# Optimization experiments

Measured on AMD Instinct MI355X. Metric: run time of the kernel, lower is better.

## Reference

```python
import jax, jax.numpy as jnp
import numpy as np

C, M, D, B, BG_KNN = 8, 2048, 2048, 256, 50
TEMP, MOMENTUM = 0.05, 0.2


def setup_inputs() -> dict:
    key = jax.random.key(0)
    k1, k2, k3, k4 = jax.random.split(key, 4)
    inputs = jax.random.normal(k1, (B, D), jnp.float32)
    inputs = inputs / jnp.linalg.norm(inputs, axis=1, keepdims=True)  # ReID feats are L2-normed
    em = jax.random.normal(k2, (C * M, D), jnp.float32)
    em = em / jnp.linalg.norm(em, axis=1, keepdims=True)  # memory rows are kept unit-norm
    targets = jax.random.randint(k3, (B,), 0, M)          # global pseudo labels in [0, M)
    cams = jax.random.randint(k4, (B,), 0, C).astype(jnp.int32)
    return {"inputs": inputs, "em": em, "targets": targets, "cams": cams, "epoch": 6}


def _loss(inputs, em_sg, targets, cams, epoch):
    em3 = em_sg.reshape(C, M, D)
    loss = jnp.zeros((), jnp.float32)
    # per-camera intra-camera cross entropy (ExemplarMemory fwd: inputs @ em.T / temp)
    for cc in range(C):
        mask = (cams == cc)
        cnt = jnp.maximum(mask.sum(), 1).astype(jnp.float32)
        logits = (inputs @ em3[cc].T) / TEMP                       # [B, M]
        logp = jax.nn.log_softmax(logits, axis=1)
        ce = -jnp.take_along_axis(logp, targets[:, None], axis=1)[:, 0]
        loss = loss + jnp.where(mask.any(), jnp.where(mask, ce, 0.0).sum() / cnt, 0.0)
    if epoch >= 5:
        sims = inputs @ em_sg.T                                    # [B, C*M]
        # positives: one proxy per camera at row target + M*c
        pos_ind = targets[:, None] + M * jnp.arange(C)[None, :]    # [B, C]
        pos_logits = jnp.take_along_axis(sims, pos_ind, axis=1) / TEMP
        masked = jax.lax.stop_gradient(sims).at[jnp.arange(B)[:, None], pos_ind].set(-1000.0)
        _, neg_ind = jax.lax.top_k(masked, BG_KNN)                 # bg_knn hard negatives
        neg_logits = jnp.take_along_axis(sims, neg_ind, axis=1) / TEMP
        cat = jnp.concatenate([pos_logits, neg_logits], axis=1)   # [B, C+BG_KNN]
        logp = jax.nn.log_softmax(cat, axis=1)
        al = -logp[:, :C].mean(axis=1)                             # weights 1/#pos on positives
        for cc in range(C):
            mask = (cams == cc)
            cnt = jnp.maximum(mask.sum(), 1).astype(jnp.float32)
            loss = loss + jnp.where(mask.any(), 0.5 * jnp.where(mask, al, 0.0).sum() / cnt, 0.0)
    return loss


def reference(inputs, em, targets, cams, epoch):
    em_sg = jax.lax.stop_gradient(em)  # memory is a buffer: no grad flows to it in torch
    loss = _loss(inputs, em_sg, targets, cams, int(epoch))
    # sequential per-sample EMA scatter update + renorm (torch does this in backward)
    rows = cams.astype(jnp.int32) * M + targets.astype(jnp.int32)
    x_sg = jax.lax.stop_gradient(inputs)

    def step(em_cur, xr):
        x, r = xr
        row = MOMENTUM * em_cur[r] + (1.0 - MOMENTUM) * x
        row = row / jnp.linalg.norm(row)
        return em_cur.at[r].set(row), None

    em_new, _ = jax.lax.scan(step, em_sg, (x_sg, rows))
    return loss, em_new
```

## Files before the change

### kernel.cpp

```cpp
#include <hip/hip_runtime.h>

#define Bn 256
#define Dk 2048
#define Cc 8
#define Mm 2048
#define Nn 16384
#define BG 50
#define INV_T 20.0f

typedef __attribute__((ext_vector_type(8))) short bf16x8;
typedef __attribute__((ext_vector_type(4))) float f32x4;

__device__ inline short f2bf(float f) {
  unsigned u = __builtin_bit_cast(unsigned, f);
  u = (u + 0x7fffu + ((u >> 16) & 1u)) >> 16;
  return (short)u;
}
__device__ inline unsigned f2ord(float f) {
  unsigned u = __builtin_bit_cast(unsigned, f);
  return (u & 0x80000000u) ? ~u : (u | 0x80000000u);
}
__device__ inline float ord2f(unsigned o) {
  unsigned u = (o & 0x80000000u) ? (o ^ 0x80000000u) : ~o;
  return __builtin_bit_cast(float, u);
}

__global__ __launch_bounds__(256) void prep_kernel(const int* __restrict__ cams,
                                                   const int* __restrict__ targets,
                                                   int* __restrict__ cnt,
                                                   int* __restrict__ rowArr,
                                                   int* __restrict__ first) {
  __shared__ int rs[Bn];
  __shared__ int lc[Cc];
  const int t = threadIdx.x;
  const int r = cams[t] * Mm + targets[t];
  rs[t] = r;
  if (t < Cc) lc[t] = 0;
  __syncthreads();
  atomicAdd(&lc[cams[t]], 1);
  __syncthreads();
  if (t < Cc) cnt[t] = lc[t];
  int fst = 1;
  for (int j = 0; j < t; ++j)
    if (rs[j] == r) fst = 0;
  rowArr[t] = r;
  first[t] = fst;
}

__global__ __launch_bounds__(256) void convert_kernel(const float* __restrict__ x,
                                                      short* __restrict__ a, int n4) {
  int i = blockIdx.x * 256 + threadIdx.x;
  if (i >= n4) return;
  float4 v = ((const float4*)x)[i];
  int row = i >> 9, j = i & 511;
  int kt = j >> 3, off = (j & 7) * 4;
  short4 h;
  h.x = f2bf(v.x); h.y = f2bf(v.y); h.z = f2bf(v.z); h.w = f2bf(v.w);
  *(short4*)(a + (size_t)kt * (Bn * 32) + row * 32 + off) = h;
}

#define SA 40
__global__ __launch_bounds__(512) void gemm_copy_kernel(const short* __restrict__ A,
                                                        const float* __restrict__ Em,
                                                        float* __restrict__ sims,
                                                        float* __restrict__ out_em) {
  __shared__ __align__(16) short As[2][Bn * SA];
  __shared__ __align__(16) short Bs[2][64 * SA];
  const int tid = threadIdx.x;
  const int nbase = blockIdx.x * 64;
  const int lane = tid & 63;
  const int w = tid >> 6, wm = w & 3, wn = w >> 2;
  const int lr = lane & 15, lq = lane >> 4;

  f32x4 acc[4][2];
#pragma unroll
  for (int mi = 0; mi < 4; ++mi)
#pragma unroll
    for (int ni = 0; ni < 2; ++ni) acc[mi][ni] = (f32x4)(0.0f);

  const int arow0 = tid >> 2, achk = (tid & 3) * 8;
  const int brow = tid >> 3, bcol = (tid & 7) * 4;
  const size_t bgo_base = (size_t)(nbase + brow) * Dk + bcol;

  uint4 aReg0, aReg1;
  float4 bReg;
  aReg0 = *(const uint4*)(A + tid * 8);
  aReg1 = *(const uint4*)(A + (tid + 512) * 8);
  bReg = *(const float4*)(Em + bgo_base);

  for (int kt = 0; kt < 64; ++kt) {
    short* as = As[kt & 1];
    short* bs = Bs[kt & 1];
    *(uint4*)(as + arow0 * SA + achk) = aReg0;
    *(uint4*)(as + (arow0 + 128) * SA + achk) = aReg1;
    short4 hb;
    hb.x = f2bf(bReg.x); hb.y = f2bf(bReg.y); hb.z = f2bf(bReg.z); hb.w = f2bf(bReg.w);
    *(short4*)(bs + brow * SA + bcol) = hb;
    {
      size_t go = bgo_base + (size_t)kt * 32;
      out_em[go + 0] = bReg.x;
      out_em[go + 1] = bReg.y;
      out_em[go + 2] = bReg.z;
      out_em[go + 3] = bReg.w;
    }
    __syncthreads();
    if (kt < 63) {
      const short* ap = A + (size_t)(kt + 1) * (Bn * 32);
      aReg0 = *(const uint4*)(ap + tid * 8);
      aReg1 = *(const uint4*)(ap + (tid + 512) * 8);
      bReg = *(const float4*)(Em + bgo_base + (size_t)(kt + 1) * 32);
    }
    bf16x8 af[4], bfr[2];
#pragma unroll
    for (int mi = 0; mi < 4; ++mi)
      af[mi] = *(const bf16x8*)(as + (wm * 64 + mi * 16 + lr) * SA + lq * 8);
#pragma unroll
    for (int ni = 0; ni < 2; ++ni)
      bfr[ni] = *(const bf16x8*)(bs + (wn * 32 + ni * 16 + lr) * SA + lq * 8);
#pragma unroll
    for (int mi = 0; mi < 4; ++mi)
#pragma unroll
      for (int ni = 0; ni < 2; ++ni)
        acc[mi][ni] = __builtin_amdgcn_mfma_f32_16x16x32_bf16(af[mi], bfr[ni], acc[mi][ni], 0, 0, 0);
  }
#pragma unroll
  for (int mi = 0; mi < 4; ++mi)
#pragma unroll
    for (int ni = 0; ni < 2; ++ni)
#pragma unroll
      for (int r = 0; r < 4; ++r) {
        int m = wm * 64 + mi * 16 + lq * 4 + r;
        int n = nbase + wn * 32 + ni * 16 + lr;
        sims[(size_t)m * Nn + n] = acc[mi][ni][r];
      }
}

__device__ inline float blockRedSumF(float v, float* red, int tid) {
#pragma unroll
  for (int off = 32; off; off >>= 1) v += __shfl_down(v, off, 64);
  if ((tid & 63) == 0) red[tid >> 6] = v;
  __syncthreads();
  float r = red[0] + red[1] + red[2] + red[3];
  __syncthreads();
  return r;
}
__device__ inline int blockRedSumI(int v, int* red, int tid) {
#pragma unroll
  for (int off = 32; off; off >>= 1) v += __shfl_down(v, off, 64);
  if ((tid & 63) == 0) red[tid >> 6] = v;
  __syncthreads();
  int r = red[0] + red[1] + red[2] + red[3];
  __syncthreads();
  return r;
}
__device__ inline float blockRedMaxF(float v, float* red, int tid) {
#pragma unroll
  for (int off = 32; off; off >>= 1) v = fmaxf(v, __shfl_down(v, off, 64));
  if ((tid & 63) == 0) red[tid >> 6] = v;
  __syncthreads();
  float r = fmaxf(fmaxf(red[0], red[1]), fmaxf(red[2], red[3]));
  __syncthreads();
  return r;
}
__device__ inline unsigned blockRedMaxU(unsigned v, unsigned* red, int tid) {
#pragma unroll
  for (int off = 32; off; off >>= 1) { unsigned o = __shfl_down(v, off, 64); v = o > v ? o : v; }
  if ((tid & 63) == 0) red[tid >> 6] = v;
  __syncthreads();
  unsigned r = red[0];
  r = red[1] > r ? red[1] : r; r = red[2] > r ? red[2] : r; r = red[3] > r ? red[3] : r;
  __syncthreads();
  return r;
}

__global__ __launch_bounds__(256) void loss_kernel(const float* __restrict__ sims,
                                                   const int* __restrict__ targets,
                                                   const int* __restrict__ cams,
                                                   const int* __restrict__ cnt,
                                                   const int* __restrict__ epoch,
                                                   float* __restrict__ lossPartial) {
  __shared__ float redf[4];
  __shared__ int redi[4];
  __shared__ unsigned redu[4];
  __shared__ unsigned pordS[Cc];
  const int b = blockIdx.x, t = threadIdx.x;

  uint4 uarr[16];
  {
    const float4* src = (const float4*)(sims + (size_t)b * Nn);
#pragma unroll
    for (int q = 0; q < 16; ++q) {
      float4 v = src[q * 256 + t];
      uarr[q].x = f2ord(v.x); uarr[q].y = f2ord(v.y);
      uarr[q].z = f2ord(v.z); uarr[q].w = f2ord(v.w);
    }
  }
  const int cam = cams[b], tgt = targets[b];
  const int cg = cnt[cam];
  const float invc = 1.0f / (float)(cg > 0 ? cg : 1);

  {
    const int owner = (tgt >> 2) & 255;
    if (t == owner) {
      const int slot = tgt & 3;
#pragma unroll
      for (int c = 0; c < Cc; ++c) {
        const int chunk = (tgt >> 10) + 2 * c;
        uint4 uc = uarr[0];
#pragma unroll
        for (int q = 1; q < 16; ++q)
          if (chunk == q) uc = uarr[q];
        unsigned po = uc.x;
        if (slot == 1) po = uc.y;
        else if (slot == 2) po = uc.z;
        else if (slot == 3) po = uc.w;
        pordS[c] = po;
      }
    }
  }
  __syncthreads();
  unsigned pord[Cc];
  float pv[Cc];
#pragma unroll
  for (int c = 0; c < Cc; ++c) { pord[c] = pordS[c]; pv[c] = ord2f(pord[c]); }

  float cv[8];
  {
    uint4 u0 = uarr[0], u1 = uarr[1];
#pragma unroll
    for (int q = 0; q < 16; ++q) {
      if (2 * cam == q) u0 = uarr[q];
      if (2 * cam + 1 == q) u1 = uarr[q];
    }
    cv[0] = ord2f(u0.x); cv[1] = ord2f(u0.y); cv[2] = ord2f(u0.z); cv[3] = ord2f(u0.w);
    cv[4] = ord2f(u1.x); cv[5] = ord2f(u1.y); cv[6] = ord2f(u1.z); cv[7] = ord2f(u1.w);
  }
  float lm = cv[0];
#pragma unroll
  for (int k = 1; k < 8; ++k) lm = fmaxf(lm, cv[k]);
  const float maxv = blockRedMaxF(lm, redf, t);
  float ls = 0.0f;
#pragma unroll
  for (int k = 0; k < 8; ++k) ls += __expf((cv[k] - maxv) * INV_T);
  const float sumexp = blockRedSumF(ls, redf, t);
  float total = (__logf(sumexp) + (maxv - pv[cam]) * INV_T) * invc;

  if (*epoch >= 5) {
    unsigned cur = 0u;
#pragma unroll 1
    for (int bit = 31; bit >= 0; --bit) {
      const unsigned cand = cur | (1u << bit);
      int c = 0;
#pragma unroll
      for (int q = 0; q < 16; ++q)
        c += (uarr[q].x >= cand) + (uarr[q].y >= cand) + (uarr[q].z >= cand) + (uarr[q].w >= cand);
      int ctot = blockRedSumI(c, redi, t);
#pragma unroll
      for (int cc2 = 0; cc2 < Cc; ++cc2) ctot -= (pord[cc2] >= cand);
      if (ctot >= BG) cur = cand;
    }
    int cg2 = 0;
#pragma unroll
    for (int q = 0; q < 16; ++q)
      cg2 += (uarr[q].x > cur) + (uarr[q].y > cur) + (uarr[q].z > cur) + (uarr[q].w > cur);
    int cgt = blockRedSumI(cg2, redi, t);
#pragma unroll
    for (int cc2 = 0; cc2 < Cc; ++cc2) cgt -= (pord[cc2] > cur);
    unsigned um = 0u;
#pragma unroll
    for (int q = 0; q < 16; ++q) {
      um = uarr[q].x > um ? uarr[q].x : um;
      um = uarr[q].y > um ? uarr[q].y : um;
      um = uarr[q].z > um ? uarr[q].z : um;
      um = uarr[q].w > um ? uarr[q].w : um;
    }
    const unsigned umax = blockRedMaxU(um, redu, t);
    const float m = ord2f(umax);
    const float v50 = ord2f(cur);
    float s = 0.0f;
#pragma unroll
    for (int q = 0; q < 16; ++q) {
      if (uarr[q].x > cur) s += __expf((ord2f(uarr[q].x) - m) * INV_T);
      if (uarr[q].y > cur) s += __expf((ord2f(uarr[q].y) - m) * INV_T);
      if (uarr[q].z > cur) s += __expf((ord2f(uarr[q].z) - m) * INV_T);
      if (uarr[q].w > cur) s += __expf((ord2f(uarr[q].w) - m) * INV_T);
    }
    float S = blockRedSumF(s, redf, t);
    float psum = 0.0f;
#pragma unroll
    for (int cc2 = 0; cc2 < Cc; ++cc2) {
      if (pord[cc2] > cur) S -= __expf((pv[cc2] - m) * INV_T);
      S += __expf((pv[cc2] - m) * INV_T);
      psum += pv[cc2];
    }
    S += (float)(BG - cgt) * __expf((v50 - m) * INV_T);
    const float lse = m * INV_T + __logf(S);
    const float al = lse - psum * (INV_T / 8.0f);
    total += 0.5f * al * invc;
  }
  if (t == 0) lossPartial[b] = total;
}

__global__ __launch_bounds__(256) void finalize_kernel(const float* __restrict__ lossPartial,
                                                       float* __restrict__ loss) {
  __shared__ float redf[4];
  const int t = threadIdx.x;
  float v = lossPartial[t];
  const float r = blockRedSumF(v, redf, t);
  if (t == 0) loss[0] = r;
}

__global__ __launch_bounds__(256) void ema_kernel(const float* __restrict__ em,
                                                  const float* __restrict__ inputs,
                                                  const int* __restrict__ rowArr,
                                                  const int* __restrict__ first,
                                                  float* __restrict__ out_em) {
  const int b = blockIdx.x, tid = threadIdx.x;
  if (!first[b]) return;
  const int r = rowArr[b];
  __shared__ int rows[Bn];
  __shared__ float red[4];
  rows[tid] = rowArr[tid];
  __syncthreads();
  float v[8];
#pragma unroll
  for (int u = 0; u < 8; ++u) v[u] = em[(size_t)r * Dk + u * 256 + tid];
  const int lane = tid & 63, w = tid >> 6;
  for (int j = b; j < Bn; ++j) {
    if (rows[j] != r) continue;
#pragma unroll
    for (int u = 0; u < 8; ++u)
      v[u] = 0.2f * v[u] + 0.8f * inputs[(size_t)j * Dk + u * 256 + tid];
    float ss = 0.0f;
#pragma unroll
    for (int u = 0; u < 8; ++u) ss += v[u] * v[u];
#pragma unroll
    for (int off = 32; off; off >>= 1) ss += __shfl_down(ss, off, 64);
    if (lane == 0) red[w] = ss;
    __syncthreads();
    const float inv = 1.0f / sqrtf(red[0] + red[1] + red[2] + red[3]);
#pragma unroll
    for (int u = 0; u < 8; ++u) v[u] *= inv;
    __syncthreads();
  }
#pragma unroll
  for (int u = 0; u < 8; ++u) out_em[(size_t)r * Dk + u * 256 + tid] = v[u];
}

extern "C" void kernel_launch(void* const* d_in, const int* in_sizes, int n_in,
                              void* d_out, int out_size, void* d_ws, size_t ws_size,
                              hipStream_t stream) {
  const float* inputs  = (const float*)d_in[0];
  const float* em      = (const float*)d_in[1];
  const int*   targets = (const int*)d_in[2];
  const int*   cams    = (const int*)d_in[3];
  const int*   epoch   = (const int*)d_in[4];
  float* loss   = (float*)d_out;
  float* out_em = (float*)d_out + 1;

  float* sims = (float*)d_ws;
  short* a16  = (short*)((char*)d_ws + (size_t)Bn * Nn * 4);
  float* lossPartial = (float*)((char*)d_ws + (size_t)Bn * Nn * 4 + (size_t)Bn * Dk * 2);
  int* ibase  = (int*)(lossPartial + Bn);
  int* cnt    = ibase;
  int* rowArr = ibase + 8;
  int* first  = ibase + 8 + Bn;

  hipLaunchKernelGGL(prep_kernel,    dim3(1),       dim3(256), 0, stream, cams, targets, cnt, rowArr, first);
  hipLaunchKernelGGL(convert_kernel, dim3(512),     dim3(256), 0, stream, inputs, a16, Bn * Dk / 4);
  hipLaunchKernelGGL(gemm_copy_kernel, dim3(Nn / 64), dim3(512), 0, stream, a16, em, sims, out_em);
  hipLaunchKernelGGL(loss_kernel,    dim3(Bn),      dim3(256), 0, stream, sims, targets, cams, cnt, epoch, lossPartial);
  hipLaunchKernelGGL(finalize_kernel, dim3(1),      dim3(256), 0, stream, lossPartial, loss);
  hipLaunchKernelGGL(ema_kernel,     dim3(Bn),      dim3(256), 0, stream, em, inputs, rowArr, first, out_em);
}
```

Before: 370.4 us.

## Load GEMM fragments directly from global memory, dropping LDS staging and barriers

The GEMM+copy kernel no longer stages A and B tiles through shared memory with double buffering and __syncthreads. Each wave now loads its MFMA fragments straight from global memory (pre-tiled bf16 A, fp32 Em converted to bf16 in registers), and the loop is unrolled by 4 so loads can be issued ahead. This removes the LDS writes, reads and per-iteration barriers. In exchange, A and B data are fetched redundantly across waves: each A fragment is read by both wn waves and each B row by all four wm waves, which raises global/L2 traffic. The out_em copy stays as a separate stream of loads and stores.

Measured after the change: 407.8 us. 10.1% more time.

```diff
diff --git a/kernel.cpp b/kernel.cpp
--- a/kernel.cpp
+++ b/kernel.cpp
@@ -59,13 +59,10 @@
   *(short4*)(a + (size_t)kt * (Bn * 32) + row * 32 + off) = h;
 }
 
-#define SA 40
 __global__ __launch_bounds__(512) void gemm_copy_kernel(const short* __restrict__ A,
                                                         const float* __restrict__ Em,
                                                         float* __restrict__ sims,
                                                         float* __restrict__ out_em) {
-  __shared__ __align__(16) short As[2][Bn * SA];
-  __shared__ __align__(16) short Bs[2][64 * SA];
   const int tid = threadIdx.x;
   const int nbase = blockIdx.x * 64;
   const int lane = tid & 63;
@@ -78,51 +75,43 @@
 #pragma unroll
     for (int ni = 0; ni < 2; ++ni) acc[mi][ni] = (f32x4)(0.0f);
 
-  const int arow0 = tid >> 2, achk = (tid & 3) * 8;
-  const int brow = tid >> 3, bcol = (tid & 7) * 4;
-  const size_t bgo_base = (size_t)(nbase + brow) * Dk + bcol;
-
-  uint4 aReg0, aReg1;
-  float4 bReg;
-  aReg0 = *(const uint4*)(A + tid * 8);
-  aReg1 = *(const uint4*)(A + (tid + 512) * 8);
-  bReg = *(const float4*)(Em + bgo_base);
-
+  const short* aP = A + (wm * 64 + lr) * 32 + lq * 8;
+  const float* bP = Em + (size_t)(nbase + wn * 32 + lr) * Dk + lq * 8;
+  const int crow = tid >> 3, ccol = (tid & 7) * 4;
+  const float* cS = Em + (size_t)(nbase + crow) * Dk + ccol;
+  float* cD = out_em + (size_t)(nbase + crow) * Dk + ccol;
+
+#pragma unroll 4
   for (int kt = 0; kt < 64; ++kt) {
-    short* as = As[kt & 1];
-    short* bs = Bs[kt & 1];
-    *(uint4*)(as + arow0 * SA + achk) = aReg0;
-    *(uint4*)(as + (arow0 + 128) * SA + achk) = aReg1;
-    short4 hb;
-    hb.x = f2bf(bReg.x); hb.y = f2bf(bReg.y); hb.z = f2bf(bReg.z); hb.w = f2bf(bReg.w);
-    *(short4*)(bs + brow * SA + bcol) = hb;
-    {
-      size_t go = bgo_base + (size_t)kt * 32;
-      out_em[go + 0] = bReg.x;
-      out_em[go + 1] = bReg.y;
-      out_em[go + 2] = bReg.z;
-      out_em[go + 3] = bReg.w;
-    }
-    __syncthreads();
-    if (kt < 63) {
-      const short* ap = A + (size_t)(kt + 1) * (Bn * 32);
-      aReg0 = *(const uint4*)(ap + tid * 8);
-      aReg1 = *(const uint4*)(ap + (tid + 512) * 8);
-      bReg = *(const float4*)(Em + bgo_base + (size_t)(kt + 1) * 32);
-    }
-    bf16x8 af[4], bfr[2];
-#pragma unroll
-    for (int mi = 0; mi < 4; ++mi)
-      af[mi] = *(const bf16x8*)(as + (wm * 64 + mi * 16 + lr) * SA + lq * 8);
-#pragma unroll
-    for (int ni = 0; ni < 2; ++ni)
-      bfr[ni] = *(const bf16x8*)(bs + (wn * 32 + ni * 16 + lr) * SA + lq * 8);
-#pragma unroll
-    for (int mi = 0; mi < 4; ++mi)
-#pragma unroll
-      for (int ni = 0; ni < 2; ++ni)
-        acc[mi][ni] = __builtin_amdgcn_mfma_f32_16x16x32_bf16(af[mi], bfr[ni], acc[mi][ni], 0, 0, 0);
-  }
+    bf16x8 a0 = *(const bf16x8*)(aP + (size_t)kt * 8192);
+    bf16x8 a1 = *(const bf16x8*)(aP + (size_t)kt * 8192 + 512);
+    bf16x8 a2 = *(const bf16x8*)(aP + (size_t)kt * 8192 + 1024);
+    bf16x8 a3 = *(const bf16x8*)(aP + (size_t)kt * 8192 + 1536);
+    float4 b00 = *(const float4*)(bP + kt * 32);
+    float4 b01 = *(const float4*)(bP + kt * 32 + 4);
+    float4 b10 = *(const float4*)(bP + 16 * Dk + kt * 32);
+    float4 b11 = *(const float4*)(bP + 16 * Dk + kt * 32 + 4);
+    float4 c = *(const float4*)(cS + kt * 32);
+
+    bf16x8 bf0, bf1;
+    bf0[0] = f2bf(b00.x); bf0[1] = f2bf(b00.y); bf0[2] = f2bf(b00.z); bf0[3] = f2bf(b00.w);
+    bf0[4] = f2bf(b01.x); bf0[5] = f2bf(b01.y); bf0[6] = f2bf(b01.z); bf0[7] = f2bf(b01.w);
+    bf1[0] = f2bf(b10.x); bf1[1] = f2bf(b10.y); bf1[2] = f2bf(b10.z); bf1[3] = f2bf(b10.w);
+    bf1[4] = f2bf(b11.x); bf1[5] = f2bf(b11.y); bf1[6] = f2bf(b11.z); bf1[7] = f2bf(b11.w);
+
+    acc[0][0] = __builtin_amdgcn_mfma_f32_16x16x32_bf16(a0, bf0, acc[0][0], 0, 0, 0);
+    acc[0][1] = __builtin_amdgcn_mfma_f32_16x16x32_bf16(a0, bf1, acc[0][1], 0, 0, 0);
+    acc[1][0] = __builtin_amdgcn_mfma_f32_16x16x32_bf16(a1, bf0, acc[1][0], 0, 0, 0);
+    acc[1][1] = __builtin_amdgcn_mfma_f32_16x16x32_bf16(a1, bf1, acc[1][1], 0, 0, 0);
+    acc[2][0] = __builtin_amdgcn_mfma_f32_16x16x32_bf16(a2, bf0, acc[2][0], 0, 0, 0);
+    acc[2][1] = __builtin_amdgcn_mfma_f32_16x16x32_bf16(a2, bf1, acc[2][1], 0, 0, 0);
+    acc[3][0] = __builtin_amdgcn_mfma_f32_16x16x32_bf16(a3, bf0, acc[3][0], 0, 0, 0);
+    acc[3][1] = __builtin_amdgcn_mfma_f32_16x16x32_bf16(a3, bf1, acc[3][1], 0, 0, 0);
+
+    float* d = cD + kt * 32;
+    d[0] = c.x; d[1] = c.y; d[2] = c.z; d[3] = c.w;
+  }
+
 #pragma unroll
   for (int mi = 0; mi < 4; ++mi)
 #pragma unroll
```
